# Optimization experiments

Measured on AMD Instinct MI355X. Metric: run time of the kernel, lower is better.

The kernel has to match this reference:

```python
import jax, jax.numpy as jnp
import numpy as np

B, C, H, W = 16, 64, 128, 128
K = 3
Z = 128


def setup_inputs() -> dict:
    key = jax.random.key(0)
    k1, k2, k3, k4 = jax.random.split(key, 4)
    x = jax.random.normal(k1, (B, C, H, W), dtype=jnp.float32)
    z = jax.random.normal(k2, (B, Z), dtype=jnp.float32)
    # generator: Linear(Z -> C*C*K*K), scaled for stable conv outputs
    gen_w = jax.random.normal(k3, (Z, C * C * K * K), dtype=jnp.float32) * 0.02
    gen_b = jax.random.normal(k4, (C * C * K * K,), dtype=jnp.float32) * 0.02
    return {"x": x, "z": z, "gen_w": gen_w, "gen_b": gen_b}


def _conv_one(xi, wi):
    # xi: [C,H,W], wi: [C_out,C_in,K,K]; 'same' padding conv, no bias
    out = jax.lax.conv_general_dilated(
        xi[None], wi, window_strides=(1, 1), padding="SAME",
        dimension_numbers=("NCHW", "OIHW", "NCHW"))
    return out[0]


def reference(x, z, gen_w, gen_b):
    # per-sample weight generation: [B, C*C*K*K] -> [B, C, C, K, K]
    weight = (z @ gen_w + gen_b).reshape(B, C, C, K, K)
    # batched per-sample convolution (replaces the python loop over batch)
    return jax.vmap(_conv_one)(x, weight)
```

## Files before the change

kernel.cpp:

```cpp
#include <hip/hip_runtime.h>
#include <hip/hip_bf16.h>

typedef __attribute__((ext_vector_type(4))) float f32x4;
typedef __attribute__((ext_vector_type(8))) short short8;

#define B_ 16
#define C_ 64
#define H_ 128
#define W_ 128
#define Z_ 128
#define IDXN (C_*C_*9)
#define NT 18

#define AS_GLOBAL(p) ((const __attribute__((address_space(1))) void*)(p))
#define AS_LDS(p)    ((__attribute__((address_space(3))) void*)(p))

__device__ __forceinline__ unsigned short f2bf(float f) {
  __hip_bfloat16 h = __float2bfloat16(f);
  return *reinterpret_cast<unsigned short*>(&h);
}

__global__ __launch_bounds__(256) void wgen_k(
    const float* __restrict__ z, const float* __restrict__ gw,
    const float* __restrict__ gb, unsigned short* __restrict__ wfrag) {
  __shared__ __align__(16) float zs[B_*Z_];
  int t = threadIdx.x;
#pragma unroll
  for (int i = 0; i < 8; ++i) zs[i*256 + t] = z[i*256 + t];
  __syncthreads();
  int lane = t & 63, bg = t >> 6;
  int b0 = bg*4;
  int idx0 = blockIdx.x*128 + lane;
  float acc[4][2];
  float bv0 = gb[idx0], bv1 = gb[idx0 + 64];
#pragma unroll
  for (int bi = 0; bi < 4; ++bi) { acc[bi][0] = bv0; acc[bi][1] = bv1; }

  for (int z0 = 0; z0 < Z_; z0 += 4) {
    float ga[4], gbv[4];
#pragma unroll
    for (int zi = 0; zi < 4; ++zi) {
      ga[zi]  = gw[(size_t)(z0+zi)*IDXN + idx0];
      gbv[zi] = gw[(size_t)(z0+zi)*IDXN + idx0 + 64];
    }
#pragma unroll
    for (int bi = 0; bi < 4; ++bi) {
      f32x4 zq = *reinterpret_cast<const f32x4*>(&zs[(b0+bi)*Z_ + z0]);
      acc[bi][0] = fmaf(zq[0], ga[0], fmaf(zq[1], ga[1], fmaf(zq[2], ga[2], fmaf(zq[3], ga[3], acc[bi][0]))));
      acc[bi][1] = fmaf(zq[0], gbv[0], fmaf(zq[1], gbv[1], fmaf(zq[2], gbv[2], fmaf(zq[3], gbv[3], acc[bi][1]))));
    }
  }
#pragma unroll
  for (int ni = 0; ni < 2; ++ni) {
    int idx = idx0 + ni*64;
    int kw = idx % 3, r1 = idx/3;
    int kh = r1 % 3, r2 = r1/3;
    int ci = r2 & 63, co = r2 >> 6;
    int k = (kh*3 + kw)*C_ + ci;
    int ts = k >> 5, kin = k & 31;
    int lm = (co & 15) | ((kin >> 3) << 4);
    int j = kin & 7, m = co >> 4;
    int base = ((ts*4 + m)*64 + lm)*8 + j;
#pragma unroll
    for (int bi = 0; bi < 4; ++bi)
      wfrag[(size_t)(b0+bi)*(NT*4*64*8) + base] = f2bf(acc[bi][ni]);
  }
}

__global__ __launch_bounds__(256) void xpose_k(
    const float* __restrict__ x, unsigned short* __restrict__ xTs) {
  __shared__ __align__(16) unsigned short lt[C_*134];
  int p = blockIdx.x;
  int b = p >> 7, h = p & 127;
  int t = threadIdx.x;
  const float* xb = x + ((size_t)b*C_*H_ + h)*W_;

  int wq = t & 31, ci0 = t >> 5;
#pragma unroll
  for (int p8 = 0; p8 < 8; ++p8) {
    int ci = ci0 + p8*8;
    f32x4 v = *reinterpret_cast<const f32x4*>(&xb[(size_t)ci*(H_*W_) + wq*4]);
    unsigned int u0 = (unsigned int)f2bf(v[0]) | ((unsigned int)f2bf(v[1]) << 16);
    unsigned int u1 = (unsigned int)f2bf(v[2]) | ((unsigned int)f2bf(v[3]) << 16);
    uint2 val; val.x = u0; val.y = u1;
    *reinterpret_cast<uint2*>(&lt[ci*134 + wq*4]) = val;
  }
  __syncthreads();

  int ci8 = t & 7, wp0 = t >> 3;
  unsigned short* dst = xTs + ((size_t)(b*H_ + h)*W_)*C_;
#pragma unroll
  for (int wi = 0; wi < 2; ++wi) {
    int wp = wp0 + wi*32;
    unsigned int q[8];
#pragma unroll
    for (int j = 0; j < 8; ++j)
      q[j] = *reinterpret_cast<const unsigned int*>(&lt[(ci8*8 + j)*134 + wp*2]);
    uint4 o0, o1;
    unsigned short* s0 = reinterpret_cast<unsigned short*>(&o0);
    unsigned short* s1 = reinterpret_cast<unsigned short*>(&o1);
#pragma unroll
    for (int j = 0; j < 8; ++j) {
      s0[j] = (unsigned short)(q[j] & 0xffffu);
      s1[j] = (unsigned short)(q[j] >> 16);
    }
    int w0 = 2*wp, w1 = 2*wp + 1;
    int sl0 = ci8 ^ ((w0 + 1) & 7);
    int sl1 = ci8 ^ ((w1 + 1) & 7);
    *reinterpret_cast<uint4*>(dst + (size_t)w0*C_ + sl0*8) = o0;
    *reinterpret_cast<uint4*>(dst + (size_t)w1*C_ + sl1*8) = o1;
  }
}

__global__ __launch_bounds__(256) void conv_k(
    const unsigned short* __restrict__ xTs,
    const unsigned short* __restrict__ wfrag,
    float* __restrict__ out) {
  __shared__ __align__(16) unsigned char xs[4*130*128];
  int orig = blockIdx.x;
  int blk = (orig & 7)*128 + (orig >> 3);
  int b = blk >> 6;
  int h0 = (blk & 63)*2;
  int tid = threadIdx.x;
  int v = tid >> 6, lane = tid & 63;

  {
    int hh = h0 - 1 + v;
    bool hv = (hh >= 0) & (hh < H_);
    unsigned char* ldsrow = xs + v*(130*128);
    if (hv) {
      if (lane < 16) {
        int s = (lane < 8) ? lane : (1024 + lane);
        uint4 zv; zv.x = 0; zv.y = 0; zv.z = 0; zv.w = 0;
        *reinterpret_cast<uint4*>(ldsrow + s*16) = zv;
      }
      const unsigned char* xrow = reinterpret_cast<const unsigned char*>(
          xTs + ((size_t)(b*H_ + hh)*W_)*C_);
#pragma unroll
      for (int it = 0; it < 16; ++it) {
        __builtin_amdgcn_global_load_lds(
            AS_GLOBAL(xrow + ((size_t)(it*64))*16 + (size_t)lane*16),
            AS_LDS(ldsrow + (8 + it*64)*16), 16, 0, 0);
      }
    } else {
      uint4 zv; zv.x = 0; zv.y = 0; zv.z = 0; zv.w = 0;
#pragma unroll
      for (int it = 0; it < 17; ++it) {
        int di = it*64 + lane;
        if (di < 1040) *reinterpret_cast<uint4*>(ldsrow + di*16) = zv;
      }
    }
  }
  __syncthreads();

  int l15 = lane & 15, lhi = lane >> 4;
  int phr = v >> 1, pw0 = (v & 1)*64;
  f32x4 acc[4][4];
#pragma unroll
  for (int mp = 0; mp < 4; ++mp)
#pragma unroll
    for (int nc = 0; nc < 4; ++nc)
      acc[mp][nc] = (f32x4){0.f, 0.f, 0.f, 0.f};

  const unsigned short* wb = wfrag + (size_t)b*(NT*4*64*8);
#pragma unroll
  for (int t = 0; t < NT; ++t) {
    int kk = t >> 1, kh = kk/3, kw = kk%3, half = t & 1;
    short8 wf[4];
#pragma unroll
    for (int nc = 0; nc < 4; ++nc)
      wf[nc] = *reinterpret_cast<const short8*>(wb + ((t*4 + nc)*64 + lane)*8);
    int chunk = half*4 + lhi;
    short8 xa[4];
#pragma unroll
    for (int mp = 0; mp < 4; ++mp) {
      int col = pw0 + mp*16 + l15 + kw;
      int addr = ((phr + kh)*130 + col)*128 + (((chunk ^ col) & 7) << 4);
      xa[mp] = *reinterpret_cast<const short8*>(&xs[addr]);
    }
#pragma unroll
    for (int mp = 0; mp < 4; ++mp)
#pragma unroll
      for (int nc = 0; nc < 4; ++nc)
        acc[mp][nc] = __builtin_amdgcn_mfma_f32_16x16x32_bf16(xa[mp], wf[nc], acc[mp][nc], 0, 0, 0);
  }

  int ph = h0 + phr;
#pragma unroll
  for (int nc = 0; nc < 4; ++nc) {
    int co = nc*16 + l15;
    float* op = out + (((size_t)b*C_ + co)*H_ + ph)*W_;
#pragma unroll
    for (int mp = 0; mp < 4; ++mp) {
      int pix = pw0 + mp*16 + lhi*4;
      *reinterpret_cast<f32x4*>(op + pix) = acc[mp][nc];
    }
  }
}

__global__ void sentinel_k(float* out, int n) {
  int i = blockIdx.x*256 + threadIdx.x;
  if (i < n) out[i] = 1.0e6f;
}

extern "C" void kernel_launch(void* const* d_in, const int* in_sizes, int n_in,
                              void* d_out, int out_size, void* d_ws, size_t ws_size,
                              hipStream_t stream) {
  const float* x  = (const float*)d_in[0];
  const float* z  = (const float*)d_in[1];
  const float* gw = (const float*)d_in[2];
  const float* gb = (const float*)d_in[3];
  float* out = (float*)d_out;

  size_t wfrag_elems = (size_t)B_*IDXN;
  size_t xT_elems    = (size_t)B_*H_*W_*C_;
  size_t need = (wfrag_elems + xT_elems)*sizeof(unsigned short);
  if (ws_size < need) {
    sentinel_k<<<(out_size + 255)/256, 256, 0, stream>>>(out, out_size);
    return;
  }
  unsigned short* wfrag = (unsigned short*)d_ws;
  unsigned short* xTs   = wfrag + wfrag_elems;

  wgen_k <<<IDXN/128, 256, 0, stream>>>(z, gw, gb, wfrag);
  xpose_k<<<B_*H_,    256, 0, stream>>>(x, xTs);
  conv_k <<<B_*(H_/2),256, 0, stream>>>(xTs, wfrag, out);
}
```

Baseline: 62.26 us.

## Fuse NCHW-to-bf16 transpose into conv kernel's LDS staging

Removes the separate transpose kernel and its bf16 workspace. The conv kernel now reads fp32 NCHW rows straight from x, converts them to bf16 and writes the swizzled channel-last layout into LDS itself. This drops one kernel launch and a full write-then-read round trip of the transposed activation through global memory. In exchange, each input row is now read by up to three conv blocks (halo rows) as fp32 rather than bf16, and the async global-to-LDS loads become register-staged loads with conversion work inside the conv kernel.

```diff
diff --git a/kernel.cpp b/kernel.cpp
--- a/kernel.cpp
+++ b/kernel.cpp
@@ -11,9 +11,6 @@
 #define Z_ 128
 #define IDXN (C_*C_*9)
 #define NT 18
-
-#define AS_GLOBAL(p) ((const __attribute__((address_space(1))) void*)(p))
-#define AS_LDS(p)    ((__attribute__((address_space(3))) void*)(p))
 
 __device__ __forceinline__ unsigned short f2bf(float f) {
   __hip_bfloat16 h = __float2bfloat16(f);
@@ -67,53 +64,8 @@
   }
 }
 
-__global__ __launch_bounds__(256) void xpose_k(
-    const float* __restrict__ x, unsigned short* __restrict__ xTs) {
-  __shared__ __align__(16) unsigned short lt[C_*134];
-  int p = blockIdx.x;
-  int b = p >> 7, h = p & 127;
-  int t = threadIdx.x;
-  const float* xb = x + ((size_t)b*C_*H_ + h)*W_;
-
-  int wq = t & 31, ci0 = t >> 5;
-#pragma unroll
-  for (int p8 = 0; p8 < 8; ++p8) {
-    int ci = ci0 + p8*8;
-    f32x4 v = *reinterpret_cast<const f32x4*>(&xb[(size_t)ci*(H_*W_) + wq*4]);
-    unsigned int u0 = (unsigned int)f2bf(v[0]) | ((unsigned int)f2bf(v[1]) << 16);
-    unsigned int u1 = (unsigned int)f2bf(v[2]) | ((unsigned int)f2bf(v[3]) << 16);
-    uint2 val; val.x = u0; val.y = u1;
-    *reinterpret_cast<uint2*>(&lt[ci*134 + wq*4]) = val;
-  }
-  __syncthreads();
-
-  int ci8 = t & 7, wp0 = t >> 3;
-  unsigned short* dst = xTs + ((size_t)(b*H_ + h)*W_)*C_;
-#pragma unroll
-  for (int wi = 0; wi < 2; ++wi) {
-    int wp = wp0 + wi*32;
-    unsigned int q[8];
-#pragma unroll
-    for (int j = 0; j < 8; ++j)
-      q[j] = *reinterpret_cast<const unsigned int*>(&lt[(ci8*8 + j)*134 + wp*2]);
-    uint4 o0, o1;
-    unsigned short* s0 = reinterpret_cast<unsigned short*>(&o0);
-    unsigned short* s1 = reinterpret_cast<unsigned short*>(&o1);
-#pragma unroll
-    for (int j = 0; j < 8; ++j) {
-      s0[j] = (unsigned short)(q[j] & 0xffffu);
-      s1[j] = (unsigned short)(q[j] >> 16);
-    }
-    int w0 = 2*wp, w1 = 2*wp + 1;
-    int sl0 = ci8 ^ ((w0 + 1) & 7);
-    int sl1 = ci8 ^ ((w1 + 1) & 7);
-    *reinterpret_cast<uint4*>(dst + (size_t)w0*C_ + sl0*8) = o0;
-    *reinterpret_cast<uint4*>(dst + (size_t)w1*C_ + sl1*8) = o1;
-  }
-}
-
 __global__ __launch_bounds__(256) void conv_k(
-    const unsigned short* __restrict__ xTs,
+    const float* __restrict__ x,
     const unsigned short* __restrict__ wfrag,
     float* __restrict__ out) {
   __shared__ __align__(16) unsigned char xs[4*130*128];
@@ -130,17 +82,32 @@
     unsigned char* ldsrow = xs + v*(130*128);
     if (hv) {
       if (lane < 16) {
-        int s = (lane < 8) ? lane : (1024 + lane);
+        int s = (lane < 8) ? lane : (1024 + lane - 8 + 8);
         uint4 zv; zv.x = 0; zv.y = 0; zv.z = 0; zv.w = 0;
         *reinterpret_cast<uint4*>(ldsrow + s*16) = zv;
       }
-      const unsigned char* xrow = reinterpret_cast<const unsigned char*>(
-          xTs + ((size_t)(b*H_ + hh)*W_)*C_);
+      const float* xrow = x + (((size_t)b*C_)*H_ + hh)*W_;
+      int w0 = 2*lane, col0 = w0 + 1, col1 = w0 + 2;
+      int g = lane >> 3;
 #pragma unroll
-      for (int it = 0; it < 16; ++it) {
-        __builtin_amdgcn_global_load_lds(
-            AS_GLOBAL(xrow + ((size_t)(it*64))*16 + (size_t)lane*16),
-            AS_LDS(ldsrow + (8 + it*64)*16), 16, 0, 0);
+      for (int c8 = 0; c8 < 8; ++c8) {
+        int chunk = (c8 + g) & 7;
+        float2 v2[8];
+#pragma unroll
+        for (int j = 0; j < 8; ++j)
+          v2[j] = *reinterpret_cast<const float2*>(xrow + (size_t)(chunk*8 + j)*(H_*W_) + w0);
+        uint4 o0, o1;
+        unsigned short* s0 = reinterpret_cast<unsigned short*>(&o0);
+        unsigned short* s1 = reinterpret_cast<unsigned short*>(&o1);
+#pragma unroll
+        for (int j = 0; j < 8; ++j) {
+          s0[j] = f2bf(v2[j].x);
+          s1[j] = f2bf(v2[j].y);
+        }
+        int a0 = col0*128 + (((chunk ^ col0) & 7) << 4);
+        int a1 = col1*128 + (((chunk ^ col1) & 7) << 4);
+        *reinterpret_cast<uint4*>(ldsrow + a0) = o0;
+        *reinterpret_cast<uint4*>(ldsrow + a1) = o1;
       }
     } else {
       uint4 zv; zv.x = 0; zv.y = 0; zv.z = 0; zv.w = 0;
@@ -213,16 +180,13 @@
   float* out = (float*)d_out;
 
   size_t wfrag_elems = (size_t)B_*IDXN;
-  size_t xT_elems    = (size_t)B_*H_*W_*C_;
-  size_t need = (wfrag_elems + xT_elems)*sizeof(unsigned short);
+  size_t need = wfrag_elems*sizeof(unsigned short);
   if (ws_size < need) {
     sentinel_k<<<(out_size + 255)/256, 256, 0, stream>>>(out, out_size);
     return;
   }
   unsigned short* wfrag = (unsigned short*)d_ws;
-  unsigned short* xTs   = wfrag + wfrag_elems;
 
   wgen_k <<<IDXN/128, 256, 0, stream>>>(z, gw, gb, wfrag);
-  xpose_k<<<B_*H_,    256, 0, stream>>>(x, xTs);
-  conv_k <<<B_*(H_/2),256, 0, stream>>>(xTs, wfrag, out);
+  conv_k <<<B_*(H_/2),256, 0, stream>>>(x, wfrag, out);
 }
```

New measurement: 50.45 us. 1.23x faster.
